# Kernel optimization log

Measured on AMD Instinct MI355X. Metric: run time of the kernel, lower is better.

The kernel has to match this reference:

```python
import jax, jax.numpy as jnp
import numpy as np

N = 100000      # nodes
E = 1200000     # edges
H = 64          # hidden_channels
L = 8           # num_layers
G = 100         # graphs in batch
ALPHA = 0.1
THETA = 0.5
EPS = 1e-5      # BatchNorm1d eps


def setup_inputs() -> dict:
    key = jax.random.key(0)
    ks = jax.random.split(key, 12)
    s = 0.05
    pos = jax.random.normal(ks[0], (N, 3), dtype=jnp.float32)
    edge_index = jax.random.randint(ks[1], (2, E), 0, N, dtype=jnp.int32)
    batch = jnp.sort(jax.random.randint(ks[2], (N,), 0, G, dtype=jnp.int32))
    return {
        "pos": pos,
        "edge_index": edge_index,
        "batch": batch,
        "lin0_w": jax.random.normal(ks[3], (3, H), dtype=jnp.float32) * s,
        "lin0_b": jnp.zeros((H,), jnp.float32),
        "conv_w": jax.random.normal(ks[4], (L, H, H), dtype=jnp.float32) * s,
        "lin1_w": jax.random.normal(ks[5], (H, H), dtype=jnp.float32) * s,
        "lin1_b": jnp.zeros((H,), jnp.float32),
        "mlp1_w": jax.random.normal(ks[6], (H, H), dtype=jnp.float32) * s,
        "mlp1_b": jnp.zeros((H,), jnp.float32),
        "bn1_g": jnp.ones((H,), jnp.float32),
        "bn1_b": jnp.zeros((H,), jnp.float32),
        "mlp2_w": jax.random.normal(ks[7], (H, H), dtype=jnp.float32) * s,
        "mlp2_b": jnp.zeros((H,), jnp.float32),
        "bn2_g": jnp.ones((H,), jnp.float32),
        "bn2_b": jnp.zeros((H,), jnp.float32),
        "out_w": jax.random.normal(ks[8], (H, 10), dtype=jnp.float32) * s,
        "out_b": jnp.zeros((10,), jnp.float32),
    }


def _bn(z, g, b):
    # BatchNorm1d, training-mode batch statistics
    mu = z.mean(axis=0)
    var = z.var(axis=0)
    return g * (z - mu) * jax.lax.rsqrt(var + EPS) + b


def reference(pos, edge_index, batch, lin0_w, lin0_b, conv_w, lin1_w, lin1_b,
              mlp1_w, mlp1_b, bn1_g, bn1_b, mlp2_w, mlp2_b, bn2_g, bn2_b,
              out_w, out_b):
    src, dst = edge_index[0], edge_index[1]
    x = jax.nn.relu(pos @ lin0_w + lin0_b)   # [N, H]
    x0 = x
    for l in range(L):
        beta = float(np.log(THETA / (l + 1) + 1.0))
        # GCN2Conv (normalize=False, shared_weights=True):
        # sum-aggregate neighbors, initial residual, identity mapping
        agg = jax.ops.segment_sum(x[src], dst, num_segments=N)   # [N, H]
        h = (1.0 - ALPHA) * agg + ALPHA * x0
        x = jax.nn.relu((1.0 - beta) * h + beta * (h @ conv_w[l]))
    x = x @ lin1_w + lin1_b
    pooled = jax.ops.segment_max(x, batch, num_segments=G)       # [G, H]
    pooled = jnp.where(jnp.isfinite(pooled), pooled, 0.0)        # guard empty segments
    h1 = jax.nn.relu(_bn(pooled @ mlp1_w + mlp1_b, bn1_g, bn1_b))
    h2 = jax.nn.relu(_bn(h1 @ mlp2_w + mlp2_b, bn2_g, bn2_b))
    logits = h2 @ out_w + out_b                                  # [G, 10]
    return jax.nn.log_softmax(logits, axis=-1)
```

## Files before the change

kernel.cpp:

```cpp
#include <hip/hip_runtime.h>
#include <math.h>

#define NNODES 100000
#define NEDGES 1200000
#define HD 64
#define NLAYERS 8
#define NGRAPH 100
#define PPART 32
#define NPART 8
#define C8 16777216.0f

typedef _Float16 f16;
typedef __attribute__((ext_vector_type(8))) _Float16 f16x8;
typedef __attribute__((ext_vector_type(4))) float f32x4;

__global__ void lin0_k(const float* __restrict__ pos, const float* __restrict__ w,
                       const float* __restrict__ b, f16* __restrict__ x0h, int total) {
    int i = blockIdx.x * blockDim.x + threadIdx.x;
    if (i >= total) return;
    int n = i >> 6, h = i & 63;
    float p0 = pos[n * 3 + 0], p1 = pos[n * 3 + 1], p2 = pos[n * 3 + 2];
    float v = fmaf(p0, w[h], fmaf(p1, w[64 + h], fmaf(p2, w[128 + h], b[h])));
    x0h[i] = (f16)fmaxf(v, 0.0f);
}

__global__ void hist_k(const int* __restrict__ dst, int* __restrict__ degp,
                       int* __restrict__ rank, int E) {
    int e = blockIdx.x * 256 + threadIdx.x;
    int p = blockIdx.x & (NPART - 1);
    if (e < E) rank[e] = atomicAdd(&degp[p * NNODES + dst[e]], 1);
}

__global__ void offs_k(const int* __restrict__ degp, int* __restrict__ poff,
                       int* __restrict__ deg, int n) {
    int d = blockIdx.x * blockDim.x + threadIdx.x;
    if (d >= n) return;
    int s = 0;
#pragma unroll
    for (int p = 0; p < NPART; ++p) {
        poff[p * n + d] = s;
        s += degp[p * n + d];
    }
    deg[d] = s;
}

__global__ void scan_part_k(const int* __restrict__ deg, int* __restrict__ bsum, int n) {
    __shared__ int s[256];
    int t = threadIdx.x;
    int i = blockIdx.x * 256 + t;
    s[t] = (i < n) ? deg[i] : 0;
    __syncthreads();
    for (int off = 128; off > 0; off >>= 1) {
        if (t < off) s[t] += s[t + off];
        __syncthreads();
    }
    if (t == 0) bsum[blockIdx.x] = s[0];
}

__global__ void scan_mid_k(const int* __restrict__ bsum, int* __restrict__ boff,
                           int nblk, int* __restrict__ roff, int n) {
    __shared__ int s[512];
    int t = threadIdx.x;
    int v = (t < nblk) ? bsum[t] : 0;
    s[t] = v;
    __syncthreads();
    for (int off = 1; off < 512; off <<= 1) {
        int u = (t >= off) ? s[t - off] : 0;
        __syncthreads();
        s[t] += u;
        __syncthreads();
    }
    if (t < nblk) boff[t] = s[t] - v;
    if (t == nblk - 1) roff[n] = s[t];
}

__global__ void scan_final_k(const int* __restrict__ deg, const int* __restrict__ boff,
                             int* __restrict__ roff, int n) {
    __shared__ int s[256];
    int t = threadIdx.x;
    int i = blockIdx.x * 256 + t;
    int v = (i < n) ? deg[i] : 0;
    s[t] = v;
    __syncthreads();
    for (int off = 1; off < 256; off <<= 1) {
        int u = (t >= off) ? s[t - off] : 0;
        __syncthreads();
        s[t] += u;
        __syncthreads();
    }
    if (i < n) roff[i] = boff[blockIdx.x] + s[t] - v;
}

__global__ void fill_k(const int* __restrict__ src, const int* __restrict__ dst,
                       const int* __restrict__ roff, const int* __restrict__ poff,
                       const int* __restrict__ rank, int* __restrict__ csr, int E) {
    int e = blockIdx.x * 256 + threadIdx.x;
    if (e < E) {
        int d = dst[e];
        int p = (e >> 8) & (NPART - 1);
        csr[roff[d] + poff[p * NNODES + d] + rank[e]] = src[e];
    }
}

__global__ void prep_k(const float* __restrict__ cw, const float* __restrict__ l1w,
                       f16* __restrict__ Bpack) {
    int t = blockIdx.x * blockDim.x + threadIdx.x;
    if (t >= 9 * 4 * 2 * 64) return;
    int mat = t >> 9, rem = t & 511;
    int ct = rem >> 7, kk = (rem >> 6) & 1, lane = rem & 63;
    int g = lane >> 4, r = lane & 15;
    f16* outp = Bpack + (size_t)t * 8;
    if (mat < 8) {
        float beta = logf(0.5f / (float)(mat + 1) + 1.0f);
        const float* W = cw + (size_t)mat * 4096;
        for (int j = 0; j < 8; ++j) {
            int row = 32 * kk + 8 * g + j;
            int col = 16 * ct + r;
            float m = beta * W[row * 64 + col];
            if (row == col) m += 1.0f - beta;
            outp[j] = (f16)(0.125f * m);
        }
    } else {
        for (int j = 0; j < 8; ++j) {
            int row = 32 * kk + 8 * g + j;
            int col = 16 * ct + r;
            outp[j] = (f16)l1w[row * 64 + col];
        }
    }
}

__global__ __launch_bounds__(256, 8) void layer_k(
    const f16* __restrict__ xin, f16* __restrict__ xout,
    const f16* __restrict__ x0, const f16* __restrict__ Bp,
    const int* __restrict__ roff, const int* __restrict__ csr,
    float x0scale, int total_waves) {
    __shared__ __align__(16) f16 Htile[4][16][72];
    const int tid   = threadIdx.x;
    const int lane  = tid & 63;
    const int wslot = tid >> 6;
    const int wid0  = (blockIdx.x * blockDim.x + tid) >> 6;
    const int ar = lane & 15, ag = lane >> 4;
    for (int tile = wid0; tile < NNODES / 16; tile += total_waves) {
        const int nbase = tile << 4;
#pragma unroll 1
        for (int i = 0; i < 16; ++i) {
            const int n = nbase + i;
            const int beg = roff[n], end = roff[n + 1];
            float x0v = (float)x0[(n << 6) + lane];
            float s0 = 0.0f, s1 = 0.0f, s2 = 0.0f, s3 = 0.0f;
            int e = beg;
            for (; e + 8 <= end; e += 8) {
                int i0 = csr[e + 0], i1 = csr[e + 1], i2 = csr[e + 2], i3 = csr[e + 3];
                int i4 = csr[e + 4], i5 = csr[e + 5], i6 = csr[e + 6], i7 = csr[e + 7];
                f16 v0 = xin[(i0 << 6) + lane];
                f16 v1 = xin[(i1 << 6) + lane];
                f16 v2 = xin[(i2 << 6) + lane];
                f16 v3 = xin[(i3 << 6) + lane];
                f16 v4 = xin[(i4 << 6) + lane];
                f16 v5 = xin[(i5 << 6) + lane];
                f16 v6 = xin[(i6 << 6) + lane];
                f16 v7 = xin[(i7 << 6) + lane];
                s0 += (float)v0; s1 += (float)v1; s2 += (float)v2; s3 += (float)v3;
                s0 += (float)v4; s1 += (float)v5; s2 += (float)v6; s3 += (float)v7;
            }
            for (; e + 4 <= end; e += 4) {
                int i0 = csr[e + 0], i1 = csr[e + 1], i2 = csr[e + 2], i3 = csr[e + 3];
                s0 += (float)xin[(i0 << 6) + lane];
                s1 += (float)xin[(i1 << 6) + lane];
                s2 += (float)xin[(i2 << 6) + lane];
                s3 += (float)xin[(i3 << 6) + lane];
            }
            for (; e < end; ++e) s0 += (float)xin[(csr[e] << 6) + lane];
            float h = fmaf(0.9f, (s0 + s1) + (s2 + s3), x0scale * x0v);
            Htile[wslot][i][lane] = (f16)h;
        }
        __builtin_amdgcn_wave_barrier();
        f16x8 a0 = *(const f16x8*)&Htile[wslot][ar][(ag << 3) + 0];
        f16x8 a1 = *(const f16x8*)&Htile[wslot][ar][(ag << 3) + 32];
#pragma unroll 1
        for (int ct = 0; ct < 4; ++ct) {
            f16x8 b0 = *(const f16x8*)(Bp + (size_t)((ct * 2 + 0) * 64 + lane) * 8);
            f16x8 b1 = *(const f16x8*)(Bp + (size_t)((ct * 2 + 1) * 64 + lane) * 8);
            f32x4 acc = {0.0f, 0.0f, 0.0f, 0.0f};
            acc = __builtin_amdgcn_mfma_f32_16x16x32_f16(a0, b0, acc, 0, 0, 0);
            acc = __builtin_amdgcn_mfma_f32_16x16x32_f16(a1, b1, acc, 0, 0, 0);
            const int col = (ct << 4) + ar;
            const int rbase = nbase + (ag << 2);
#pragma unroll
            for (int j = 0; j < 4; ++j) {
                xout[((rbase + j) << 6) + col] = (f16)fmaxf(acc[j], 0.0f);
            }
        }
        __builtin_amdgcn_wave_barrier();
    }
}

__global__ __launch_bounds__(256, 8) void lin1_k(
    const f16* __restrict__ xin, f16* __restrict__ yout,
    const f16* __restrict__ Bp, int nblocks) {
    const int lane  = threadIdx.x & 63;
    const int wslot = threadIdx.x >> 6;
    const f16x8 b0 = *(const f16x8*)(Bp + (size_t)((wslot * 2 + 0) * 64 + lane) * 8);
    const f16x8 b1 = *(const f16x8*)(Bp + (size_t)((wslot * 2 + 1) * 64 + lane) * 8);
    const int ar = lane & 15, ag = lane >> 4;
    for (int tile = blockIdx.x; tile < NNODES / 16; tile += nblocks) {
        const int nbase = tile << 4;
        f16x8 a0 = *(const f16x8*)(xin + ((size_t)(nbase + ar) << 6) + (ag << 3));
        f16x8 a1 = *(const f16x8*)(xin + ((size_t)(nbase + ar) << 6) + (ag << 3) + 32);
        f32x4 acc = {0.0f, 0.0f, 0.0f, 0.0f};
        acc = __builtin_amdgcn_mfma_f32_16x16x32_f16(a0, b0, acc, 0, 0, 0);
        acc = __builtin_amdgcn_mfma_f32_16x16x32_f16(a1, b1, acc, 0, 0, 0);
        const int col = (wslot << 4) + ar;
        const int rbase = nbase + (ag << 2);
#pragma unroll
        for (int j = 0; j < 4; ++j) {
            yout[((rbase + j) << 6) + col] = (f16)acc[j];
        }
    }
}

__device__ __forceinline__ int lbound(const int* __restrict__ a, int n, int v) {
    int lo = 0, hi = n;
    while (lo < hi) { int mid = (lo + hi) >> 1; if (a[mid] < v) lo = mid + 1; else hi = mid; }
    return lo;
}

__global__ __launch_bounds__(256, 8) void segmax_k(
    const f16* __restrict__ y, const int* __restrict__ batch,
    float* __restrict__ pmax) {
    __shared__ float wm[4][64];
    const int tid   = threadIdx.x;
    const int lane  = tid & 63;
    const int wslot = tid >> 6;
    const int g = blockIdx.x / PPART, part = blockIdx.x % PPART;
    const int lo = lbound(batch, NNODES, g);
    const int hi = lbound(batch, NNODES, g + 1);
    const int cnt = hi - lo;
    const int qlo = lo + (cnt * part) / PPART;
    const int qhi = lo + (cnt * (part + 1)) / PPART;
    float vmax = -INFINITY;
    for (int n = qlo + wslot; n < qhi; n += 4)
        vmax = fmaxf(vmax, (float)y[(n << 6) + lane]);
    wm[wslot][lane] = vmax;
    __syncthreads();
    if (tid < 64) {
        float m = fmaxf(fmaxf(wm[0][tid], wm[1][tid]), fmaxf(wm[2][tid], wm[3][tid]));
        pmax[blockIdx.x * 64 + tid] = m;
    }
}

__global__ void poolcomb_k(const float* __restrict__ pmax,
                           const float* __restrict__ bvec,
                           float* __restrict__ pooled) {
    int i = blockIdx.x * blockDim.x + threadIdx.x;
    if (i >= NGRAPH * 64) return;
    int g = i >> 6, lane = i & 63;
    float m = -INFINITY;
    for (int p = 0; p < PPART; ++p)
        m = fmaxf(m, pmax[(PPART * g + p) * 64 + lane]);
    pooled[i] = fmaf(C8, m, bvec[lane]);
}

__global__ __launch_bounds__(256) void head_k(
    const float* __restrict__ pooled,
    const float* __restrict__ m1w, const float* __restrict__ m1b,
    const float* __restrict__ g1, const float* __restrict__ be1,
    const float* __restrict__ m2w, const float* __restrict__ m2b,
    const float* __restrict__ g2, const float* __restrict__ be2,
    const float* __restrict__ ow, const float* __restrict__ ob,
    float* __restrict__ out) {
    __shared__ float A[NGRAPH * 64];
    __shared__ float B[NGRAPH * 64];
    __shared__ float mu[64], rs[64];
    __shared__ float LG[NGRAPH * 10];
    int t = threadIdx.x;
    for (int i = t; i < NGRAPH * 64; i += 256) {
        float f = pooled[i];
        if (!isfinite(f)) f = 0.0f;
        A[i] = f;
    }
    __syncthreads();
    for (int i = t; i < NGRAPH * 64; i += 256) {
        int g = i >> 6, j = i & 63;
        float acc = m1b[j];
        for (int k = 0; k < 64; ++k) acc = fmaf(A[(g << 6) + k], m1w[k * 64 + j], acc);
        B[i] = acc;
    }
    __syncthreads();
    if (t < 64) {
        float sm = 0.0f, sq = 0.0f;
        for (int g = 0; g < NGRAPH; ++g) { float z = B[g * 64 + t]; sm += z; sq += z * z; }
        float m = sm * (1.0f / NGRAPH);
        float var = sq * (1.0f / NGRAPH) - m * m;
        mu[t] = m; rs[t] = rsqrtf(var + 1e-5f);
    }
    __syncthreads();
    for (int i = t; i < NGRAPH * 64; i += 256) {
        int j = i & 63;
        float z = fmaf((B[i] - mu[j]) * rs[j], g1[j], be1[j]);
        A[i] = fmaxf(z, 0.0f);
    }
    __syncthreads();
    for (int i = t; i < NGRAPH * 64; i += 256) {
        int g = i >> 6, j = i & 63;
        float acc = m2b[j];
        for (int k = 0; k < 64; ++k) acc = fmaf(A[(g << 6) + k], m2w[k * 64 + j], acc);
        B[i] = acc;
    }
    __syncthreads();
    if (t < 64) {
        float sm = 0.0f, sq = 0.0f;
        for (int g = 0; g < NGRAPH; ++g) { float z = B[g * 64 + t]; sm += z; sq += z * z; }
        float m = sm * (1.0f / NGRAPH);
        float var = sq * (1.0f / NGRAPH) - m * m;
        mu[t] = m; rs[t] = rsqrtf(var + 1e-5f);
    }
    __syncthreads();
    for (int i = t; i < NGRAPH * 64; i += 256) {
        int j = i & 63;
        float z = fmaf((B[i] - mu[j]) * rs[j], g2[j], be2[j]);
        A[i] = fmaxf(z, 0.0f);
    }
    __syncthreads();
    for (int i = t; i < NGRAPH * 10; i += 256) {
        int g = i / 10, j = i - g * 10;
        float acc = ob[j];
        for (int k = 0; k < 64; ++k) acc = fmaf(A[(g << 6) + k], ow[k * 10 + j], acc);
        LG[i] = acc;
    }
    __syncthreads();
    if (t < NGRAPH) {
        float m = -1e30f;
        for (int j = 0; j < 10; ++j) m = fmaxf(m, LG[t * 10 + j]);
        float s = 0.0f;
        for (int j = 0; j < 10; ++j) s += expf(LG[t * 10 + j] - m);
        float lse = m + logf(s);
        for (int j = 0; j < 10; ++j) out[t * 10 + j] = LG[t * 10 + j] - lse;
    }
}

extern "C" void kernel_launch(void* const* d_in, const int* in_sizes, int n_in,
                              void* d_out, int out_size, void* d_ws, size_t ws_size,
                              hipStream_t stream) {
    const float* pos   = (const float*)d_in[0];
    const int*   eidx  = (const int*)d_in[1];
    const int*   batch = (const int*)d_in[2];
    const float* l0w   = (const float*)d_in[3];
    const float* l0b   = (const float*)d_in[4];
    const float* cw    = (const float*)d_in[5];
    const float* l1w   = (const float*)d_in[6];
    const float* l1b   = (const float*)d_in[7];
    const float* m1w   = (const float*)d_in[8];
    const float* m1b   = (const float*)d_in[9];
    const float* g1    = (const float*)d_in[10];
    const float* b1    = (const float*)d_in[11];
    const float* m2w   = (const float*)d_in[12];
    const float* m2b   = (const float*)d_in[13];
    const float* g2    = (const float*)d_in[14];
    const float* b2    = (const float*)d_in[15];
    const float* ow    = (const float*)d_in[16];
    const float* ob    = (const float*)d_in[17];
    float* out = (float*)d_out;
    const int* src = eidx;
    const int* dst = eidx + NEDGES;

    size_t off = 0;
    auto alloc = [&](size_t bytes) -> void* {
        void* p = (char*)d_ws + off;
        off += (bytes + 255) & ~(size_t)255;
        return p;
    };
    f16*   x0h    = (f16*)alloc((size_t)NNODES * 64 * 2);
    f16*   xA     = (f16*)alloc((size_t)NNODES * 64 * 2);
    f16*   xB     = (f16*)alloc((size_t)NNODES * 64 * 2);
    int*   deg    = (int*)alloc((size_t)NNODES * 4);
    int*   degp   = (int*)alloc((size_t)NPART * NNODES * 4);
    int*   poff   = (int*)alloc((size_t)NPART * NNODES * 4);
    int*   roff   = (int*)alloc((size_t)(NNODES + 1) * 4);
    const int NBLK = (NNODES + 255) / 256;
    int*   bsum   = (int*)alloc((size_t)NBLK * 4);
    int*   boff   = (int*)alloc((size_t)NBLK * 4);
    int*   csr    = (int*)alloc((size_t)NEDGES * 4);
    float* pooled = (float*)alloc((size_t)NGRAPH * 64 * 4);
    float* pmax   = (float*)alloc((size_t)NGRAPH * PPART * 64 * 4);
    f16*   Bpack  = (f16*)alloc((size_t)9 * 4 * 2 * 64 * 8 * 2);
    int*   rank   = (int*)xB;

    hipMemsetAsync(degp, 0, (size_t)NPART * NNODES * 4, stream);
    {
        int total = NNODES * 64;
        lin0_k<<<(total + 255) / 256, 256, 0, stream>>>(pos, l0w, l0b, x0h, total);
    }
    hist_k<<<(NEDGES + 255) / 256, 256, 0, stream>>>(dst, degp, rank, NEDGES);
    offs_k<<<NBLK, 256, 0, stream>>>(degp, poff, deg, NNODES);
    scan_part_k<<<NBLK, 256, 0, stream>>>(deg, bsum, NNODES);
    scan_mid_k<<<1, 512, 0, stream>>>(bsum, boff, NBLK, roff, NNODES);
    scan_final_k<<<NBLK, 256, 0, stream>>>(deg, boff, roff, NNODES);
    fill_k<<<(NEDGES + 255) / 256, 256, 0, stream>>>(src, dst, roff, poff, rank, csr, NEDGES);
    prep_k<<<(9 * 4 * 2 * 64 + 255) / 256, 256, 0, stream>>>(cw, l1w, Bpack);

    const int LBLOCKS = 2048;
    const int TW = LBLOCKS * 256 / 64;
    const f16* cur = x0h;
    for (int l = 0; l < NLAYERS; ++l) {
        float x0scale = (float)(0.1 * ldexp(1.0, -3 * l));
        f16* nxt = (l & 1) ? xB : xA;
        layer_k<<<LBLOCKS, 256, 0, stream>>>(cur, nxt, x0h,
                                             Bpack + (size_t)l * 4 * 2 * 64 * 8,
                                             roff, csr, x0scale, TW);
        cur = nxt;
    }
    f16* l1out = (cur == xA) ? xB : xA;
    lin1_k<<<LBLOCKS, 256, 0, stream>>>(cur, l1out,
                                        Bpack + (size_t)8 * 4 * 2 * 64 * 8, LBLOCKS);
    segmax_k<<<NGRAPH * PPART, 256, 0, stream>>>(l1out, batch, pmax);
    poolcomb_k<<<(NGRAPH * 64 + 255) / 256, 256, 0, stream>>>(pmax, l1b, pooled);
    head_k<<<1, 256, 0, stream>>>(pooled, m1w, m1b, g1, b1, m2w, m2b, g2, b2, ow, ob, out);
}
```

Before: 565.1 us.

## Share a 16-node tile across the block's four waves in GCN layer kernel

```diff
diff --git a/kernel.cpp b/kernel.cpp
--- a/kernel.cpp
+++ b/kernel.cpp
@@ -133,18 +133,18 @@
     const f16* __restrict__ xin, f16* __restrict__ xout,
     const f16* __restrict__ x0, const f16* __restrict__ Bp,
     const int* __restrict__ roff, const int* __restrict__ csr,
-    float x0scale, int total_waves) {
-    __shared__ __align__(16) f16 Htile[4][16][72];
+    float x0scale, int nblocks) {
+    __shared__ __align__(16) f16 Htile[16][72];
     const int tid   = threadIdx.x;
     const int lane  = tid & 63;
     const int wslot = tid >> 6;
-    const int wid0  = (blockIdx.x * blockDim.x + tid) >> 6;
-    const int ar = lane & 15, ag = lane >> 4;
-    for (int tile = wid0; tile < NNODES / 16; tile += total_waves) {
+    const f16x8 b0 = *(const f16x8*)(Bp + (size_t)((wslot * 2 + 0) * 64 + lane) * 8);
+    const f16x8 b1 = *(const f16x8*)(Bp + (size_t)((wslot * 2 + 1) * 64 + lane) * 8);
+    for (int tile = blockIdx.x; tile < NNODES / 16; tile += nblocks) {
         const int nbase = tile << 4;
 #pragma unroll 1
-        for (int i = 0; i < 16; ++i) {
-            const int n = nbase + i;
+        for (int i = 0; i < 4; ++i) {
+            const int n = nbase + (wslot << 2) + i;
             const int beg = roff[n], end = roff[n + 1];
             float x0v = (float)x0[(n << 6) + lane];
             float s0 = 0.0f, s1 = 0.0f, s2 = 0.0f, s3 = 0.0f;
@@ -172,26 +172,22 @@
             }
             for (; e < end; ++e) s0 += (float)xin[(csr[e] << 6) + lane];
             float h = fmaf(0.9f, (s0 + s1) + (s2 + s3), x0scale * x0v);
-            Htile[wslot][i][lane] = (f16)h;
+            Htile[(wslot << 2) + i][lane] = (f16)h;
         }
-        __builtin_amdgcn_wave_barrier();
-        f16x8 a0 = *(const f16x8*)&Htile[wslot][ar][(ag << 3) + 0];
-        f16x8 a1 = *(const f16x8*)&Htile[wslot][ar][(ag << 3) + 32];
-#pragma unroll 1
-        for (int ct = 0; ct < 4; ++ct) {
-            f16x8 b0 = *(const f16x8*)(Bp + (size_t)((ct * 2 + 0) * 64 + lane) * 8);
-            f16x8 b1 = *(const f16x8*)(Bp + (size_t)((ct * 2 + 1) * 64 + lane) * 8);
-            f32x4 acc = {0.0f, 0.0f, 0.0f, 0.0f};
-            acc = __builtin_amdgcn_mfma_f32_16x16x32_f16(a0, b0, acc, 0, 0, 0);
-            acc = __builtin_amdgcn_mfma_f32_16x16x32_f16(a1, b1, acc, 0, 0, 0);
-            const int col = (ct << 4) + ar;
-            const int rbase = nbase + (ag << 2);
+        __syncthreads();
+        const int ar = lane & 15, ag = lane >> 4;
+        f16x8 a0 = *(const f16x8*)&Htile[ar][(ag << 3) + 0];
+        f16x8 a1 = *(const f16x8*)&Htile[ar][(ag << 3) + 32];
+        f32x4 acc = {0.0f, 0.0f, 0.0f, 0.0f};
+        acc = __builtin_amdgcn_mfma_f32_16x16x32_f16(a0, b0, acc, 0, 0, 0);
+        acc = __builtin_amdgcn_mfma_f32_16x16x32_f16(a1, b1, acc, 0, 0, 0);
+        const int col = (wslot << 4) + ar;
+        const int rbase = nbase + (ag << 2);
 #pragma unroll
-            for (int j = 0; j < 4; ++j) {
-                xout[((rbase + j) << 6) + col] = (f16)fmaxf(acc[j], 0.0f);
-            }
+        for (int j = 0; j < 4; ++j) {
+            xout[((rbase + j) << 6) + col] = (f16)fmaxf(acc[j], 0.0f);
         }
-        __builtin_amdgcn_wave_barrier();
+        __syncthreads();
     }
 }
 
@@ -400,14 +396,13 @@
     prep_k<<<(9 * 4 * 2 * 64 + 255) / 256, 256, 0, stream>>>(cw, l1w, Bpack);
 
     const int LBLOCKS = 2048;
-    const int TW = LBLOCKS * 256 / 64;
     const f16* cur = x0h;
     for (int l = 0; l < NLAYERS; ++l) {
         float x0scale = (float)(0.1 * ldexp(1.0, -3 * l));
         f16* nxt = (l & 1) ? xB : xA;
         layer_k<<<LBLOCKS, 256, 0, stream>>>(cur, nxt, x0h,
                                              Bpack + (size_t)l * 4 * 2 * 64 * 8,
-                                             roff, csr, x0scale, TW);
+                                             roff, csr, x0scale, LBLOCKS);
         cur = nxt;
     }
     f16* l1out = (cur == xA) ? xB : xA;
```

After: 546.9 us. 1.03x faster.
